# Kernel optimization log

Hardware: AMD Instinct MI355X
Metric: run time of the kernel (lower is better)

Reference implementation:

```python
import jax, jax.numpy as jnp
import numpy as np
from jax import lax

B, T, V, E, H = 64, 512, 32000, 256, 512
NT, C = 12, 10
PAD, BOS, EOS = 0, 10, 11
NEG = -10000.0


def setup_inputs() -> dict:
    key = jax.random.key(0)
    ks = jax.random.split(key, 16)
    x = jax.random.randint(ks[0], (B, T), 1, V)
    lengths = jax.random.randint(ks[1], (B,), T // 2, T + 1)
    x = jnp.where(jnp.arange(T)[None, :] < lengths[:, None], x, 0)

    s = 0.05
    emb = jax.random.normal(ks[2], (V, E), jnp.float32) * 0.02
    emb = emb.at[PAD].set(0.0)  # padding_idx=0
    w_ih_f = jax.random.normal(ks[3], (4 * H, E), jnp.float32) * s
    w_hh_f = jax.random.normal(ks[4], (4 * H, H), jnp.float32) * s
    b_f = jax.random.normal(ks[5], (4 * H,), jnp.float32) * s
    w_ih_b = jax.random.normal(ks[6], (4 * H, E), jnp.float32) * s
    w_hh_b = jax.random.normal(ks[7], (4 * H, H), jnp.float32) * s
    b_b = jax.random.normal(ks[8], (4 * H,), jnp.float32) * s
    fc_w = jax.random.normal(ks[9], (NT, 2 * H), jnp.float32) * s
    fc_b = jax.random.normal(ks[10], (NT,), jnp.float32) * s
    fc2_w = jax.random.normal(ks[11], (C, 2 * H), jnp.float32) * s
    fc2_b = jax.random.normal(ks[12], (C,), jnp.float32) * s
    trans = jax.random.normal(ks[13], (NT, NT), jnp.float32) * 0.1
    # CRF structural constraints (no transition into BOS, out of EOS; pad rules)
    trans = trans.at[:, BOS].set(NEG).at[EOS, :].set(NEG)
    trans = trans.at[PAD, :].set(NEG).at[PAD, EOS].set(0.0).at[PAD, PAD].set(0.0)
    return dict(x=x, emb=emb, w_ih_f=w_ih_f, w_hh_f=w_hh_f, b_f=b_f,
                w_ih_b=w_ih_b, w_hh_b=w_hh_b, b_b=b_b,
                fc_w=fc_w, fc_b=fc_b, fc2_w=fc2_w, fc2_b=fc2_b, trans=trans)


def _lstm(inputs, mask, w_ih, w_hh, b, reverse):
    # inputs [B,T,E], mask [B,T] float. Mask-aware packed-LSTM semantics:
    # state frozen on pads, outputs zeroed on pads.
    Bc = inputs.shape[0]
    Hc = w_hh.shape[1]
    def step(carry, xm):
        h, c = carry
        xt, mt = xm  # [B,E], [B]
        gates = xt @ w_ih.T + h @ w_hh.T + b
        i, f, g, o = jnp.split(gates, 4, axis=-1)  # torch gate order i,f,g,o
        i, f, o = jax.nn.sigmoid(i), jax.nn.sigmoid(f), jax.nn.sigmoid(o)
        g = jnp.tanh(g)
        c_new = f * c + i * g
        h_new = o * jnp.tanh(c_new)
        m = mt[:, None]
        return (m * h_new + (1 - m) * h, m * c_new + (1 - m) * c), m * h_new
    init = (jnp.zeros((Bc, Hc), inputs.dtype), jnp.zeros((Bc, Hc), inputs.dtype))
    xs = (inputs.transpose(1, 0, 2), mask.T)
    (hT, _), outs = lax.scan(step, init, xs, reverse=reverse)
    return outs.transpose(1, 0, 2), hT  # [B,T,H], [B,H]


def _viterbi(emissions, mask, trans):
    # emissions [B,T,NT], mask [B,T] float
    nT = trans.shape[0]
    alphas0 = trans[BOS, :][None, :] + emissions[:, 0]  # [B,NT]
    ident = jnp.arange(nT)[None, :]
    def step(alphas, inp):
        e_t, m_t = inp  # [B,NT], [B]
        scores = alphas[:, :, None] + trans[None, :, :]  # [B, prev, cur]
        best = jnp.max(scores, axis=1) + e_t
        bp = jnp.argmax(scores, axis=1)  # [B,NT]
        m = m_t[:, None]
        alphas = m * best + (1 - m) * alphas
        bp = jnp.where(m_t[:, None] > 0, bp, ident)  # identity passthrough on pads
        return alphas, bp
    xs = (emissions[:, 1:].transpose(1, 0, 2), mask[:, 1:].T)
    alphas, bps = lax.scan(step, alphas0, xs)  # bps [T-1,B,NT]
    final = alphas + trans[:, EOS][None, :]
    score = jnp.max(final, axis=-1)  # [B]
    last_tag = jnp.argmax(final, axis=-1)  # [B]
    def back(tag, bp_t):
        prev = jnp.take_along_axis(bp_t, tag[:, None], axis=1)[:, 0]
        return prev, tag
    first_tag, rest = lax.scan(back, last_tag, bps, reverse=True)
    path = jnp.concatenate([first_tag[None], rest], axis=0).T  # [B,T]
    path = jnp.where(mask > 0, path, PAD)
    return score, path


def reference(x, emb, w_ih_f, w_hh_f, b_f, w_ih_b, w_hh_b, b_b,
              fc_w, fc_b, fc2_w, fc2_b, trans):
    mask = (x != PAD).astype(jnp.float32)  # [B,T]
    fmap = emb[x]  # [B,T,E]
    h_fwd, hT_f = _lstm(fmap, mask, w_ih_f, w_hh_f, b_f, reverse=False)
    h_bwd, hT_b = _lstm(fmap, mask, w_ih_b, w_hh_b, b_b, reverse=True)
    hiddens = jnp.concatenate([h_fwd, h_bwd], axis=-1)  # [B,T,2H]
    last_hidden = jnp.concatenate([hT_f, hT_b], axis=-1)  # [B,2H]
    emissions = hiddens @ fc_w.T + fc_b  # [B,T,NT]
    class_probs = jax.nn.softmax(last_hidden @ fc2_w.T + fc2_b, axis=-1)
    score, path = _viterbi(emissions, mask, trans)
    return score, path, class_probs
```

## Files before the change

kernel.cpp:

```cpp
#include <hip/hip_runtime.h>
#include <stdint.h>
#include <math.h>

typedef __attribute__((ext_vector_type(8))) short bf16x8;
typedef __attribute__((ext_vector_type(4))) float f32x4;
typedef __attribute__((ext_vector_type(4))) unsigned short us4;
typedef __attribute__((ext_vector_type(4))) unsigned int ui4;

constexpr size_t OFF_FLAGS  = 0;
constexpr size_t OFF_RING_H = 4096;
constexpr size_t OFF_RING_M = OFF_RING_H + 262144;
constexpr size_t OFF_RING_L = OFF_RING_M + 262144;
constexpr size_t OFF_MASK   = OFF_RING_L + 262144;
constexpr size_t OFF_XE_H   = OFF_MASK + 131072;
constexpr size_t OFF_XE_L   = OFF_XE_H + 16777216;
constexpr size_t OFF_HSEQ   = OFF_XE_L + 16777216;
constexpr size_t OFF_HLAST  = OFF_HSEQ + 134217728;
constexpr size_t OFF_EMIS   = OFF_HLAST + 262144;

__device__ __forceinline__ unsigned short f2bf(float f) {
  unsigned u = __float_as_uint(f);
  unsigned r = 0x7fffu + ((u >> 16) & 1u);
  return (unsigned short)((u + r) >> 16);
}
__device__ __forceinline__ float bf2f(unsigned short h) {
  return __uint_as_float(((unsigned)h) << 16);
}
__device__ __forceinline__ void split2(float v, unsigned short &a, unsigned short &b) {
  a = f2bf(v); b = f2bf(v - bf2f(a));
}
__device__ __forceinline__ void split3(float v, unsigned short &a, unsigned short &b, unsigned short &c) {
  a = f2bf(v); float r = v - bf2f(a);
  b = f2bf(r); float r2 = r - bf2f(b);
  c = f2bf(r2);
}
__device__ __forceinline__ float sigm(float x) {
  float e = expf(-fabsf(x));
  float s = 1.0f / (1.0f + e);
  return x >= 0.0f ? s : 1.0f - s;
}
__device__ __forceinline__ f32x4 mfma16(bf16x8 a, bf16x8 b, f32x4 c) {
  return __builtin_amdgcn_mfma_f32_16x16x32_bf16(a, b, c, 0, 0, 0);
}
__device__ __forceinline__ unsigned long long ald64(const unsigned short* p) {
  return __hip_atomic_load((const unsigned long long*)p, __ATOMIC_RELAXED, __HIP_MEMORY_SCOPE_AGENT);
}
__device__ __forceinline__ void ast32(unsigned int* p, unsigned v) {
  __hip_atomic_store(p, v, __ATOMIC_RELAXED, __HIP_MEMORY_SCOPE_AGENT);
}
__device__ __forceinline__ bf16x8 ring_frag(const unsigned short* base, size_t o) {
  union { bf16x8 v; unsigned long long q[2]; } u;
  u.q[0] = ald64(base + o);
  u.q[1] = ald64(base + o + 4);
  return u.v;
}

__global__ __launch_bounds__(256) void prep_k(const int* __restrict__ x,
                                              const float* __restrict__ emb,
                                              char* __restrict__ ws)
{
  const int bid = blockIdx.x, tid = threadIdx.x;
  if (bid < 8192) {
    const int gi = bid * 256 + tid;
    const int row = gi >> 6;
    const int k = (gi & 63) * 4;
    const int b = row >> 9, t = row & 511;
    const int xid = x[row];
    const float4 v = *(const float4*)(emb + (size_t)xid * 256 + k);
    float vv[4] = {v.x, v.y, v.z, v.w};
    us4 H, L;
    #pragma unroll
    for (int j = 0; j < 4; ++j) {
      unsigned short hj, lj;
      split2(vv[j], hj, lj);
      H[j] = hj; L[j] = lj;
    }
    const size_t o = ((size_t)t * 64 + b) * 256 + k;
    *(us4*)((unsigned short*)(ws + OFF_XE_H) + o) = H;
    *(us4*)((unsigned short*)(ws + OFF_XE_L) + o) = L;
  } else if (bid < 8320) {
    const int gi = (bid - 8192) * 256 + tid;
    const int b = gi >> 9, t = gi & 511;
    ((float*)(ws + OFF_MASK))[t * 64 + b] = (x[gi] != 0) ? 1.0f : 0.0f;
  } else if (bid < 8512) {
    const int gi = (bid - 8320) * 256 + tid;
    ui4 z = {0u, 0u, 0u, 0u};
    ((ui4*)(ws + OFF_RING_H))[gi] = z;
  } else {
    ((int*)(ws + OFF_FLAGS))[tid] = 0;
  }
}

__global__ __launch_bounds__(256, 1) void lstm_k(
    const float* __restrict__ wih_f, const float* __restrict__ whh_f, const float* __restrict__ b_f,
    const float* __restrict__ wih_b, const float* __restrict__ whh_b, const float* __restrict__ b_b,
    char* __restrict__ ws)
{
  int* flags = (int*)(ws + OFF_FLAGS);
  unsigned short* ringH = (unsigned short*)(ws + OFF_RING_H);
  unsigned short* ringM = (unsigned short*)(ws + OFF_RING_M);
  unsigned short* ringL = (unsigned short*)(ws + OFF_RING_L);
  const float* maskf = (const float*)(ws + OFF_MASK);
  const unsigned short* xeH = (const unsigned short*)(ws + OFF_XE_H);
  const unsigned short* xeL = (const unsigned short*)(ws + OFF_XE_L);
  float* hseq  = (float*)(ws + OFF_HSEQ);
  float* hlast = (float*)(ws + OFF_HLAST);

  const int bid = blockIdx.x, tid = threadIdx.x;
  const int dir = bid & 1;
  const int mg  = (bid >> 1) & 3;
  const int ng  = bid >> 3;
  int* gflags = flags + (dir * 4 + mg) * 32;

  const float* whh  = dir ? whh_b : whh_f;
  const float* wih  = dir ? wih_b : wih_f;
  const float* bias = dir ? b_b  : b_f;

  const int kh = tid >> 6, lane = tid & 63;
  const int quad = lane >> 4, n16 = lane & 15;
  const int bRow = mg * 16 + n16;

  bf16x8 bhh[4][4][3];
  bf16x8 bhx[2][4][2];
  #pragma unroll
  for (int ni = 0; ni < 4; ++ni) {
    const int grow = ni * 512 + ng * 16 + n16;
    const float* hrow = whh + (size_t)grow * 512;
    const float* xrow = wih + (size_t)grow * 256;
    #pragma unroll
    for (int kt = 0; kt < 4; ++kt) {
      const int k = (4 * kt + kh) * 32 + quad * 8;
      union { bf16x8 v; unsigned short s[8]; } H, M, L;
      #pragma unroll
      for (int j = 0; j < 8; ++j) split3(hrow[k + j], H.s[j], M.s[j], L.s[j]);
      bhh[kt][ni][0] = H.v; bhh[kt][ni][1] = M.v; bhh[kt][ni][2] = L.v;
    }
    #pragma unroll
    for (int xi = 0; xi < 2; ++xi) {
      const int k = (2 * kh + xi) * 32 + quad * 8;
      union { bf16x8 v; unsigned short s[8]; } H, L;
      #pragma unroll
      for (int j = 0; j < 8; ++j) split2(xrow[k + j], H.s[j], L.s[j]);
      bhx[xi][ni][0] = H.v; bhx[xi][ni][1] = L.v;
    }
  }

  const int rowU = tid >> 4, hcU = tid & 15;
  const int bU = mg * 16 + rowU;
  const int hcol = ng * 16 + hcU;
  const float bI = bias[hcol];
  const float bF = bias[512 + hcol];
  const float bG = bias[1024 + hcol];
  const float bO = bias[1536 + hcol];
  float cstate = 0.0f, hcarry = 0.0f;

  __shared__ float gbuf[4][16][65];

  #pragma unroll 1
  for (int t = 0; t < 512; ++t) {
    const int tau = dir ? (511 - t) : t;
    f32x4 acc[4];
    const f32x4 z4 = {0.f, 0.f, 0.f, 0.f};
    #pragma unroll
    for (int ni = 0; ni < 4; ++ni) acc[ni] = z4;

    #pragma unroll
    for (int xi = 0; xi < 2; ++xi) {
      const int kx = (2 * kh + xi) * 32 + quad * 8;
      const size_t o = ((size_t)tau * 64 + bRow) * 256 + kx;
      bf16x8 aH = *(const bf16x8*)(xeH + o);
      bf16x8 aL = *(const bf16x8*)(xeL + o);
      #pragma unroll
      for (int ni = 0; ni < 4; ++ni) {
        f32x4 a = acc[ni];
        a = mfma16(aH, bhx[xi][ni][0], a);
        a = mfma16(aH, bhx[xi][ni][1], a);
        a = mfma16(aL, bhx[xi][ni][0], a);
        a = mfma16(aL, bhx[xi][ni][1], a);
        acc[ni] = a;
      }
    }

    if (tid < 32) {
      while (__hip_atomic_load(&gflags[tid], __ATOMIC_RELAXED, __HIP_MEMORY_SCOPE_AGENT) < t)
        __builtin_amdgcn_s_sleep(1);
    }
    __syncthreads();

    const int p = t & 1;
    bf16x8 rf[4][3];
    {
      const size_t rb = (((size_t)p * 2 + dir) * 64 + bRow) * 512;
      #pragma unroll
      for (int kt = 0; kt < 4; ++kt) {
        const size_t o = rb + (4 * kt + kh) * 32 + quad * 8;
        rf[kt][0] = ring_frag(ringH, o);
        rf[kt][1] = ring_frag(ringM, o);
        rf[kt][2] = ring_frag(ringL, o);
      }
    }
    #pragma unroll
    for (int kt = 0; kt < 4; ++kt) {
      #pragma unroll
      for (int ni = 0; ni < 4; ++ni) {
        f32x4 a = acc[ni];
        a = mfma16(rf[kt][0], bhh[kt][ni][0], a);
        a = mfma16(rf[kt][0], bhh[kt][ni][1], a);
        a = mfma16(rf[kt][1], bhh[kt][ni][0], a);
        a = mfma16(rf[kt][0], bhh[kt][ni][2], a);
        a = mfma16(rf[kt][1], bhh[kt][ni][1], a);
        a = mfma16(rf[kt][2], bhh[kt][ni][0], a);
        acc[ni] = a;
      }
    }

    #pragma unroll
    for (int ni = 0; ni < 4; ++ni)
      #pragma unroll
      for (int r = 0; r < 4; ++r)
        gbuf[kh][quad * 4 + r][ni * 16 + n16] = acc[ni][r];
    __syncthreads();

    const float gi = gbuf[0][rowU][hcU]      + gbuf[1][rowU][hcU]      + gbuf[2][rowU][hcU]      + gbuf[3][rowU][hcU]      + bI;
    const float gf = gbuf[0][rowU][16 + hcU] + gbuf[1][rowU][16 + hcU] + gbuf[2][rowU][16 + hcU] + gbuf[3][rowU][16 + hcU] + bF;
    const float gg = gbuf[0][rowU][32 + hcU] + gbuf[1][rowU][32 + hcU] + gbuf[2][rowU][32 + hcU] + gbuf[3][rowU][32 + hcU] + bG;
    const float go = gbuf[0][rowU][48 + hcU] + gbuf[1][rowU][48 + hcU] + gbuf[2][rowU][48 + hcU] + gbuf[3][rowU][48 + hcU] + bO;
    const float m = maskf[tau * 64 + bU];
    const float iv = sigm(gi), fv = sigm(gf), gv = tanhf(gg), ov = sigm(go);
    const float cn = fv * cstate + iv * gv;
    const float hn = ov * tanhf(cn);
    const bool mm = (m > 0.5f);
    cstate = mm ? cn : cstate;
    hcarry = mm ? hn : hcarry;

    hseq[(((size_t)dir * 64 + bU) * 512 + tau) * 512 + hcol] = mm ? hn : 0.0f;
    {
      unsigned short hb, mb, lb;
      split3(hcarry, hb, mb, lb);
      const int hbo = __shfl_xor((int)hb, 1);
      const int mbo = __shfl_xor((int)mb, 1);
      const int lbo = __shfl_xor((int)lb, 1);
      if ((tid & 1) == 0) {
        const size_t ri = (((size_t)(1 - p) * 2 + dir) * 64 + bU) * 512 + hcol;
        const size_t ui = ri >> 1;
        ast32((unsigned int*)ringH + ui, (unsigned)(unsigned short)hb | ((unsigned)(unsigned short)hbo << 16));
        ast32((unsigned int*)ringM + ui, (unsigned)(unsigned short)mb | ((unsigned)(unsigned short)mbo << 16));
        ast32((unsigned int*)ringL + ui, (unsigned)(unsigned short)lb | ((unsigned)(unsigned short)lbo << 16));
      }
    }
    __syncthreads();
    if (tid == 0) {
      __hip_atomic_store(&gflags[ng], t + 1, __ATOMIC_RELAXED, __HIP_MEMORY_SCOPE_AGENT);
    }
  }

  hlast[((size_t)dir * 64 + bU) * 512 + hcol] = hcarry;
}

__global__ __launch_bounds__(256) void emis_k(const float* __restrict__ fc_w,
                                              const float* __restrict__ fc_b,
                                              char* __restrict__ ws)
{
  __shared__ __align__(16) float fw[12 * 1024];
  __shared__ float fb[12];
  const int tid = threadIdx.x;
  for (int i = tid; i < 12 * 1024; i += 256) fw[i] = fc_w[i];
  if (tid < 12) fb[tid] = fc_b[tid];
  __syncthreads();
  const int row = blockIdx.x * 256 + tid;
  const int b = row >> 9, tau = row & 511;
  const float* hs = (const float*)(ws + OFF_HSEQ);
  double acc[12];
  #pragma unroll
  for (int n = 0; n < 12; ++n) acc[n] = (double)fb[n];
  #pragma unroll 1
  for (int d = 0; d < 2; ++d) {
    const float4* hp = (const float4*)(hs + (((size_t)d * 64 + b) * 512 + tau) * 512);
    const float* fwd = fw + d * 512;
    for (int k4 = 0; k4 < 128; ++k4) {
      const float4 hv = hp[k4];
      #pragma unroll
      for (int n = 0; n < 12; ++n) {
        const float4 wv = *(const float4*)(fwd + n * 1024 + k4 * 4);
        acc[n] += (double)hv.x * wv.x + (double)hv.y * wv.y
                + (double)hv.z * wv.z + (double)hv.w * wv.w;
      }
    }
  }
  float* em = (float*)(ws + OFF_EMIS);
  #pragma unroll
  for (int n = 0; n < 12; ++n) em[(size_t)row * 12 + n] = (float)acc[n];
}

__global__ __launch_bounds__(64) void viterbi_k(const float* __restrict__ trans,
                                                char* __restrict__ ws,
                                                float* __restrict__ out)
{
  const int b = blockIdx.x, lane = threadIdx.x;
  const float* eb = (const float*)(ws + OFF_EMIS) + (size_t)b * 6144;
  const float* maskf = (const float*)(ws + OFF_MASK);
  __shared__ float se[6144];
  __shared__ float sm[512];
  __shared__ unsigned char bp[512][12];
  for (int i = lane; i < 6144; i += 64) se[i] = eb[i];
  for (int i = lane; i < 512; i += 64) sm[i] = maskf[i * 64 + b];
  __syncthreads();
  const bool act = lane < 12;
  float tr[12];
  #pragma unroll
  for (int i = 0; i < 12; ++i) tr[i] = act ? trans[i * 12 + lane] : 0.0f;
  float alpha = act ? (trans[120 + lane] + se[lane]) : -3.0e38f;
  for (int t = 1; t < 512; ++t) {
    const float m = sm[t];
    float best = -3.0e38f; int bpi = 0;
    #pragma unroll
    for (int i = 0; i < 12; ++i) {
      const float s = __shfl(alpha, i) + tr[i];
      if (s > best) { best = s; bpi = i; }
    }
    const float ev = act ? se[t * 12 + lane] : 0.0f;
    if (m > 0.5f) alpha = best + ev; else bpi = lane;
    if (act) bp[t][lane] = (unsigned char)bpi;
  }
  const float fin = act ? (alpha + trans[lane * 12 + 11]) : -3.0e38f;
  float bestf = -3.0e38f; int bt = 0;
  #pragma unroll
  for (int j = 0; j < 12; ++j) {
    const float v = __shfl(fin, j);
    if (v > bestf) { bestf = v; bt = j; }
  }
  __syncthreads();
  if (lane == 0) {
    out[b] = bestf;
    int tag = bt;
    for (int t = 511; t >= 1; --t) {
      out[64 + (size_t)b * 512 + t] = (sm[t] > 0.5f) ? (float)tag : 0.0f;
      tag = bp[t][tag];
    }
    out[64 + (size_t)b * 512] = (float)tag;
  }
}

__global__ __launch_bounds__(64) void cls_k(const float* __restrict__ fc2_w,
                                            const float* __restrict__ fc2_b,
                                            char* __restrict__ ws,
                                            float* __restrict__ out)
{
  const int b = blockIdx.x, lane = threadIdx.x;
  const float* hl = (const float*)(ws + OFF_HLAST);
  float acc[10];
  #pragma unroll
  for (int c = 0; c < 10; ++c) acc[c] = 0.0f;
  #pragma unroll 1
  for (int kk = 0; kk < 16; ++kk) {
    const int k = lane * 16 + kk;
    const float hv = (k < 512) ? hl[(size_t)b * 512 + k]
                               : hl[((size_t)(64 + b)) * 512 + (k - 512)];
    #pragma unroll
    for (int c = 0; c < 10; ++c) acc[c] += hv * fc2_w[c * 1024 + k];
  }
  #pragma unroll
  for (int c = 0; c < 10; ++c) {
    #pragma unroll
    for (int off = 32; off >= 1; off >>= 1)
      acc[c] += __shfl_down(acc[c], off);
  }
  if (lane == 0) {
    float lg[10];
    float mx = -3.0e38f;
    #pragma unroll
    for (int c = 0; c < 10; ++c) { lg[c] = acc[c] + fc2_b[c]; mx = fmaxf(mx, lg[c]); }
    float s = 0.0f;
    #pragma unroll
    for (int c = 0; c < 10; ++c) { lg[c] = expf(lg[c] - mx); s += lg[c]; }
    const float inv = 1.0f / s;
    #pragma unroll
    for (int c = 0; c < 10; ++c) out[32832 + b * 10 + c] = lg[c] * inv;
  }
}

extern "C" void kernel_launch(void* const* d_in, const int* in_sizes, int n_in,
                              void* d_out, int out_size, void* d_ws, size_t ws_size,
                              hipStream_t stream)
{
  (void)in_sizes; (void)n_in; (void)out_size; (void)ws_size;
  const int*   x      = (const int*)d_in[0];
  const float* emb    = (const float*)d_in[1];
  const float* wih_f  = (const float*)d_in[2];
  const float* whh_f  = (const float*)d_in[3];
  const float* b_f    = (const float*)d_in[4];
  const float* wih_b  = (const float*)d_in[5];
  const float* whh_b  = (const float*)d_in[6];
  const float* b_b    = (const float*)d_in[7];
  const float* fc_w   = (const float*)d_in[8];
  const float* fc_b   = (const float*)d_in[9];
  const float* fc2_w  = (const float*)d_in[10];
  const float* fc2_b  = (const float*)d_in[11];
  const float* trans  = (const float*)d_in[12];
  char* ws = (char*)d_ws;
  float* out = (float*)d_out;

  prep_k<<<dim3(8513), dim3(256), 0, stream>>>(x, emb, ws);
  lstm_k<<<dim3(256), dim3(256), 0, stream>>>(wih_f, whh_f, b_f, wih_b, whh_b, b_b, ws);
  emis_k<<<dim3(128), dim3(256), 0, stream>>>(fc_w, fc_b, ws);
  cls_k<<<dim3(64), dim3(64), 0, stream>>>(fc2_w, fc2_b, ws, out);
  viterbi_k<<<dim3(64), dim3(64), 0, stream>>>(trans, ws, out);
}
```

Measured before the change: 2.817 ms.

## Replace per-step flag barrier with tagged 64-bit ring entries and deeper ring

The hidden-state exchange between blocks now packs a step tag together with the hi/mid/lo bf16 split into one 64-bit word, written with a single atomic store. Consumers spin on the ring entries until the tags match the current step, which removes the per-step flag wait and the trailing __syncthreads plus flag store. The ring grows to 8 slots with a coarse flag check every 4 steps to prevent overrun, gbuf is double-buffered, and the accumulators are split into two chains for more MFMA ILP. The risks are heavier polling traffic on global memory, a larger ring to zero in prep, and correctness that depends on relaxed atomics and tag wraparound.

New measurement: 4.913 ms. 1.74x slower.

```diff
diff --git a/kernel.cpp b/kernel.cpp
--- a/kernel.cpp
+++ b/kernel.cpp
@@ -8,10 +8,8 @@
 typedef __attribute__((ext_vector_type(4))) unsigned int ui4;
 
 constexpr size_t OFF_FLAGS  = 0;
-constexpr size_t OFF_RING_H = 4096;
-constexpr size_t OFF_RING_M = OFF_RING_H + 262144;
-constexpr size_t OFF_RING_L = OFF_RING_M + 262144;
-constexpr size_t OFF_MASK   = OFF_RING_L + 262144;
+constexpr size_t OFF_RING   = 4096;
+constexpr size_t OFF_MASK   = OFF_RING + 4194304;
 constexpr size_t OFF_XE_H   = OFF_MASK + 131072;
 constexpr size_t OFF_XE_L   = OFF_XE_H + 16777216;
 constexpr size_t OFF_HSEQ   = OFF_XE_L + 16777216;
@@ -42,17 +40,11 @@
 __device__ __forceinline__ f32x4 mfma16(bf16x8 a, bf16x8 b, f32x4 c) {
   return __builtin_amdgcn_mfma_f32_16x16x32_bf16(a, b, c, 0, 0, 0);
 }
-__device__ __forceinline__ unsigned long long ald64(const unsigned short* p) {
-  return __hip_atomic_load((const unsigned long long*)p, __ATOMIC_RELAXED, __HIP_MEMORY_SCOPE_AGENT);
-}
-__device__ __forceinline__ void ast32(unsigned int* p, unsigned v) {
+__device__ __forceinline__ unsigned long long ald64(const unsigned long long* p) {
+  return __hip_atomic_load(p, __ATOMIC_RELAXED, __HIP_MEMORY_SCOPE_AGENT);
+}
+__device__ __forceinline__ void ast64(unsigned long long* p, unsigned long long v) {
   __hip_atomic_store(p, v, __ATOMIC_RELAXED, __HIP_MEMORY_SCOPE_AGENT);
-}
-__device__ __forceinline__ bf16x8 ring_frag(const unsigned short* base, size_t o) {
-  union { bf16x8 v; unsigned long long q[2]; } u;
-  u.q[0] = ald64(base + o);
-  u.q[1] = ald64(base + o + 4);
-  return u.v;
 }
 
 __global__ __launch_bounds__(256) void prep_k(const int* __restrict__ x,
@@ -82,10 +74,10 @@
     const int gi = (bid - 8192) * 256 + tid;
     const int b = gi >> 9, t = gi & 511;
     ((float*)(ws + OFF_MASK))[t * 64 + b] = (x[gi] != 0) ? 1.0f : 0.0f;
-  } else if (bid < 8512) {
+  } else if (bid < 9344) {
     const int gi = (bid - 8320) * 256 + tid;
     ui4 z = {0u, 0u, 0u, 0u};
-    ((ui4*)(ws + OFF_RING_H))[gi] = z;
+    ((ui4*)(ws + OFF_RING))[gi] = z;
   } else {
     ((int*)(ws + OFF_FLAGS))[tid] = 0;
   }
@@ -97,9 +89,7 @@
     char* __restrict__ ws)
 {
   int* flags = (int*)(ws + OFF_FLAGS);
-  unsigned short* ringH = (unsigned short*)(ws + OFF_RING_H);
-  unsigned short* ringM = (unsigned short*)(ws + OFF_RING_M);
-  unsigned short* ringL = (unsigned short*)(ws + OFF_RING_L);
+  unsigned long long* ringT = (unsigned long long*)(ws + OFF_RING);
   const float* maskf = (const float*)(ws + OFF_MASK);
   const unsigned short* xeH = (const unsigned short*)(ws + OFF_XE_H);
   const unsigned short* xeL = (const unsigned short*)(ws + OFF_XE_L);
@@ -154,15 +144,16 @@
   const float bO = bias[1536 + hcol];
   float cstate = 0.0f, hcarry = 0.0f;
 
-  __shared__ float gbuf[4][16][65];
+  __shared__ float gbuf[2][4][16][65];
 
   #pragma unroll 1
   for (int t = 0; t < 512; ++t) {
     const int tau = dir ? (511 - t) : t;
-    f32x4 acc[4];
+    const int par = t & 1;
+    f32x4 aA[4], aB[4];
     const f32x4 z4 = {0.f, 0.f, 0.f, 0.f};
     #pragma unroll
-    for (int ni = 0; ni < 4; ++ni) acc[ni] = z4;
+    for (int ni = 0; ni < 4; ++ni) { aA[ni] = z4; aB[ni] = z4; }
 
     #pragma unroll
     for (int xi = 0; xi < 2; ++xi) {
@@ -172,59 +163,69 @@
       bf16x8 aL = *(const bf16x8*)(xeL + o);
       #pragma unroll
       for (int ni = 0; ni < 4; ++ni) {
-        f32x4 a = acc[ni];
+        f32x4 a = (xi == 0) ? aA[ni] : aB[ni];
         a = mfma16(aH, bhx[xi][ni][0], a);
         a = mfma16(aH, bhx[xi][ni][1], a);
         a = mfma16(aL, bhx[xi][ni][0], a);
         a = mfma16(aL, bhx[xi][ni][1], a);
-        acc[ni] = a;
-      }
-    }
-
-    if (tid < 32) {
-      while (__hip_atomic_load(&gflags[tid], __ATOMIC_RELAXED, __HIP_MEMORY_SCOPE_AGENT) < t)
-        __builtin_amdgcn_s_sleep(1);
+        if (xi == 0) aA[ni] = a; else aB[ni] = a;
+      }
+    }
+
+    if ((t & 3) == 0 && t != 0) {
+      if (tid < 32) {
+        while (__hip_atomic_load(&gflags[tid], __ATOMIC_RELAXED, __HIP_MEMORY_SCOPE_AGENT) < t - 1)
+          __builtin_amdgcn_s_sleep(1);
+      }
+    }
+
+    const size_t rb = (((size_t)(t & 7) * 2 + dir) * 64 + bRow) * 512;
+    const unsigned texp = (unsigned)t & 0xffffu;
+    #pragma unroll
+    for (int kt = 0; kt < 4; ++kt) {
+      const size_t o = rb + (4 * kt + kh) * 32 + quad * 8;
+      unsigned long long w[8];
+      for (;;) {
+        #pragma unroll
+        for (int j = 0; j < 8; ++j) w[j] = ald64(ringT + o + j);
+        unsigned bad = 0;
+        #pragma unroll
+        for (int j = 0; j < 8; ++j) bad |= ((unsigned)w[j] ^ texp) & 0xffffu;
+        if (!__any((int)bad)) break;
+      }
+      union { bf16x8 v; unsigned short s[8]; } H, M, L;
+      #pragma unroll
+      for (int j = 0; j < 8; ++j) {
+        H.s[j] = (unsigned short)(w[j] >> 16);
+        M.s[j] = (unsigned short)(w[j] >> 32);
+        L.s[j] = (unsigned short)(w[j] >> 48);
+      }
+      #pragma unroll
+      for (int ni = 0; ni < 4; ++ni) {
+        f32x4 a = (kt & 1) ? aB[ni] : aA[ni];
+        a = mfma16(H.v, bhh[kt][ni][0], a);
+        a = mfma16(H.v, bhh[kt][ni][1], a);
+        a = mfma16(M.v, bhh[kt][ni][0], a);
+        a = mfma16(H.v, bhh[kt][ni][2], a);
+        a = mfma16(M.v, bhh[kt][ni][1], a);
+        a = mfma16(L.v, bhh[kt][ni][0], a);
+        if (kt & 1) aB[ni] = a; else aA[ni] = a;
+      }
+    }
+
+    #pragma unroll
+    for (int ni = 0; ni < 4; ++ni) {
+      const f32x4 s = aA[ni] + aB[ni];
+      #pragma unroll
+      for (int r = 0; r < 4; ++r)
+        gbuf[par][kh][quad * 4 + r][ni * 16 + n16] = s[r];
     }
     __syncthreads();
 
-    const int p = t & 1;
-    bf16x8 rf[4][3];
-    {
-      const size_t rb = (((size_t)p * 2 + dir) * 64 + bRow) * 512;
-      #pragma unroll
-      for (int kt = 0; kt < 4; ++kt) {
-        const size_t o = rb + (4 * kt + kh) * 32 + quad * 8;
-        rf[kt][0] = ring_frag(ringH, o);
-        rf[kt][1] = ring_frag(ringM, o);
-        rf[kt][2] = ring_frag(ringL, o);
-      }
-    }
-    #pragma unroll
-    for (int kt = 0; kt < 4; ++kt) {
-      #pragma unroll
-      for (int ni = 0; ni < 4; ++ni) {
-        f32x4 a = acc[ni];
-        a = mfma16(rf[kt][0], bhh[kt][ni][0], a);
-        a = mfma16(rf[kt][0], bhh[kt][ni][1], a);
-        a = mfma16(rf[kt][1], bhh[kt][ni][0], a);
-        a = mfma16(rf[kt][0], bhh[kt][ni][2], a);
-        a = mfma16(rf[kt][1], bhh[kt][ni][1], a);
-        a = mfma16(rf[kt][2], bhh[kt][ni][0], a);
-        acc[ni] = a;
-      }
-    }
-
-    #pragma unroll
-    for (int ni = 0; ni < 4; ++ni)
-      #pragma unroll
-      for (int r = 0; r < 4; ++r)
-        gbuf[kh][quad * 4 + r][ni * 16 + n16] = acc[ni][r];
-    __syncthreads();
-
-    const float gi = gbuf[0][rowU][hcU]      + gbuf[1][rowU][hcU]      + gbuf[2][rowU][hcU]      + gbuf[3][rowU][hcU]      + bI;
-    const float gf = gbuf[0][rowU][16 + hcU] + gbuf[1][rowU][16 + hcU] + gbuf[2][rowU][16 + hcU] + gbuf[3][rowU][16 + hcU] + bF;
-    const float gg = gbuf[0][rowU][32 + hcU] + gbuf[1][rowU][32 + hcU] + gbuf[2][rowU][32 + hcU] + gbuf[3][rowU][32 + hcU] + bG;
-    const float go = gbuf[0][rowU][48 + hcU] + gbuf[1][rowU][48 + hcU] + gbuf[2][rowU][48 + hcU] + gbuf[3][rowU][48 + hcU] + bO;
+    const float gi = gbuf[par][0][rowU][hcU]      + gbuf[par][1][rowU][hcU]      + gbuf[par][2][rowU][hcU]      + gbuf[par][3][rowU][hcU]      + bI;
+    const float gf = gbuf[par][0][rowU][16 + hcU] + gbuf[par][1][rowU][16 + hcU] + gbuf[par][2][rowU][16 + hcU] + gbuf[par][3][rowU][16 + hcU] + bF;
+    const float gg = gbuf[par][0][rowU][32 + hcU] + gbuf[par][1][rowU][32 + hcU] + gbuf[par][2][rowU][32 + hcU] + gbuf[par][3][rowU][32 + hcU] + bG;
+    const float go = gbuf[par][0][rowU][48 + hcU] + gbuf[par][1][rowU][48 + hcU] + gbuf[par][2][rowU][48 + hcU] + gbuf[par][3][rowU][48 + hcU] + bO;
     const float m = maskf[tau * 64 + bU];
     const float iv = sigm(gi), fv = sigm(gf), gv = tanhf(gg), ov = sigm(go);
     const float cn = fv * cstate + iv * gv;
@@ -237,20 +238,14 @@
     {
       unsigned short hb, mb, lb;
       split3(hcarry, hb, mb, lb);
-      const int hbo = __shfl_xor((int)hb, 1);
-      const int mbo = __shfl_xor((int)mb, 1);
-      const int lbo = __shfl_xor((int)lb, 1);
-      if ((tid & 1) == 0) {
-        const size_t ri = (((size_t)(1 - p) * 2 + dir) * 64 + bU) * 512 + hcol;
-        const size_t ui = ri >> 1;
-        ast32((unsigned int*)ringH + ui, (unsigned)(unsigned short)hb | ((unsigned)(unsigned short)hbo << 16));
-        ast32((unsigned int*)ringM + ui, (unsigned)(unsigned short)mb | ((unsigned)(unsigned short)mbo << 16));
-        ast32((unsigned int*)ringL + ui, (unsigned)(unsigned short)lb | ((unsigned)(unsigned short)lbo << 16));
-      }
-    }
-    __syncthreads();
-    if (tid == 0) {
-      __hip_atomic_store(&gflags[ng], t + 1, __ATOMIC_RELAXED, __HIP_MEMORY_SCOPE_AGENT);
+      const unsigned long long wv = (unsigned long long)((t + 1) & 0xffff)
+                                  | ((unsigned long long)hb << 16)
+                                  | ((unsigned long long)mb << 32)
+                                  | ((unsigned long long)lb << 48);
+      ast64(ringT + (((size_t)((t + 1) & 7) * 2 + dir) * 64 + bU) * 512 + hcol, wv);
+    }
+    if ((t & 3) == 3 && tid == 0) {
+      __hip_atomic_store(&gflags[ng], t, __ATOMIC_RELAXED, __HIP_MEMORY_SCOPE_AGENT);
     }
   }
 
@@ -400,7 +395,7 @@
   char* ws = (char*)d_ws;
   float* out = (float*)d_out;
 
-  prep_k<<<dim3(8513), dim3(256), 0, stream>>>(x, emb, ws);
+  prep_k<<<dim3(9345), dim3(256), 0, stream>>>(x, emb, ws);
   lstm_k<<<dim3(256), dim3(256), 0, stream>>>(wih_f, whh_f, b_f, wih_b, whh_b, b_b, ws);
   emis_k<<<dim3(128), dim3(256), 0, stream>>>(fc_w, fc_b, ws);
   cls_k<<<dim3(64), dim3(64), 0, stream>>>(fc2_w, fc2_b, ws, out);
```
